# Kernel optimization log

Hardware: AMD Instinct MI355X
Metric: run time of the kernel (lower is better)

Reference implementation:

```python
import jax, jax.numpy as jnp
import numpy as np

N, C, H, W = 8, 64, 256, 256
HO, WO = 256, 256


def setup_inputs() -> dict:
    key = jax.random.key(0)
    kx, kg = jax.random.split(key)
    x = jax.random.normal(kx, (N, C, H, W), dtype=jnp.float32)
    # normalized sampling coords in [-1, 1], last dim = (x, y)
    grid = jax.random.uniform(kg, (N, HO, WO, 2), dtype=jnp.float32, minval=-1.0, maxval=1.0)
    return {"x": x, "grid": grid}


def reference(x, grid):
    # Bilinear grid sample, align_corners=True, border-clamped indices
    # x: [N, C, H, W]; grid: [N, Ho, Wo, 2] in [-1, 1]
    n, c, h, w = x.shape
    ix = (grid[..., 0] + 1.0) * 0.5 * (w - 1)  # [N, Ho, Wo] unnormalized x coord
    iy = (grid[..., 1] + 1.0) * 0.5 * (h - 1)

    x0f = jnp.floor(ix)
    y0f = jnp.floor(iy)
    wx1 = ix - x0f  # frac weights
    wy1 = iy - y0f
    wx0 = 1.0 - wx1
    wy0 = 1.0 - wy1

    x0 = jnp.clip(x0f, 0, w - 1).astype(jnp.int32)
    x1 = jnp.clip(x0f + 1.0, 0, w - 1).astype(jnp.int32)
    y0 = jnp.clip(y0f, 0, h - 1).astype(jnp.int32)
    y1 = jnp.clip(y0f + 1.0, 0, h - 1).astype(jnp.int32)

    xt = jnp.transpose(x, (0, 2, 3, 1))  # [N, H, W, C] for channels-last gather
    b = jnp.arange(n)[:, None, None]  # [N, 1, 1] batch index

    def gather(yi, xi):
        return xt[b, yi, xi]  # [N, Ho, Wo, C]

    out = (gather(y0, x0) * (wy0 * wx0)[..., None]
           + gather(y0, x1) * (wy0 * wx1)[..., None]
           + gather(y1, x0) * (wy1 * wx0)[..., None]
           + gather(y1, x1) * (wy1 * wx1)[..., None])
    return jnp.transpose(out, (0, 3, 1, 2))  # [N, C, Ho, Wo]
```

## Files before the change

kernel.cpp:

```cpp
#include <hip/hip_runtime.h>
#include <hip/hip_bf16.h>


constexpr int N = 8, C = 64, H = 256, W = 256, HO = 256, WO = 256;
constexpr int NPIX = N * HO * WO;
constexpr int PLANE = H * W;
constexpr size_t XT_BYTES = (size_t)N * C * PLANE * sizeof(float);

__global__ __launch_bounds__(256) void transpose_kernel(
    const float* __restrict__ x, float* __restrict__ xt) {
  __shared__ float tile[64][65];
  int tx = threadIdx.x;
  int ty = threadIdx.y;
  int tileIdx = blockIdx.x;
  int n = tileIdx >> 10;
  int pixb = (tileIdx & 1023) << 6;

  const float* xn = x + (size_t)n * C * PLANE;
#pragma unroll
  for (int k = 0; k < 16; ++k) {
    int c = (k << 2) + ty;
    tile[c][tx] = __builtin_nontemporal_load(&xn[(size_t)c * PLANE + pixb + tx]);
  }
  __syncthreads();
  float* xtn = xt + ((size_t)n * PLANE + pixb) * C;
#pragma unroll
  for (int k = 0; k < 16; ++k) {
    int p = (k << 2) + ty;
    xtn[(size_t)p * C + tx] = tile[tx][p];
  }
}

__global__ __launch_bounds__(256) void sample_kernel(
    const float* __restrict__ xt, const float* __restrict__ grid,
    float* __restrict__ out) {
  __shared__ float tile[4][64][33];
  __shared__ float4 wts[4][64];
  __shared__ int bs[4][64];

  int lane = threadIdx.x & 63;
  int wid = threadIdx.x >> 6;
  int gwave = blockIdx.x * 4 + wid;
  int pixb = gwave << 6;
  int p_idx = pixb + lane;
  int n = p_idx >> 16;

  float2 g = ((const float2*)grid)[p_idx];
  float ix = (g.x + 1.0f) * 0.5f * (float)(W - 1);
  float iy = (g.y + 1.0f) * 0.5f * (float)(H - 1);
  float x0f = floorf(ix), y0f = floorf(iy);
  float fx = ix - x0f, fy = iy - y0f;
  float cx0 = fminf(fmaxf(x0f,        0.f), (float)(W - 1));
  float cx1 = fminf(fmaxf(x0f + 1.f,  0.f), (float)(W - 1));
  float cy0 = fminf(fmaxf(y0f,        0.f), (float)(H - 1));
  float cy1 = fminf(fmaxf(y0f + 1.f,  0.f), (float)(H - 1));
  int x0 = (int)cx0, x1 = (int)cx1, y0 = (int)cy0, y1 = (int)cy1;
  int xl = min(x0, W - 2), yl = min(y0, H - 2);
  float wx0 = 1.f - fx, wx1 = fx, wy0 = 1.f - fy, wy1 = fy;
  float wxl = (x0 == xl ? wx0 : 0.f) + (x1 == xl ? wx1 : 0.f);
  float wxh = (x0 == xl + 1 ? wx0 : 0.f) + (x1 == xl + 1 ? wx1 : 0.f);
  float wyl = (y0 == yl ? wy0 : 0.f) + (y1 == yl ? wy1 : 0.f);
  float wyh = (y0 == yl + 1 ? wy0 : 0.f) + (y1 == yl + 1 ? wy1 : 0.f);
  wts[wid][lane] = make_float4(wyl * wxl, wyl * wxh, wyh * wxl, wyh * wxh);
  bs[wid][lane] = ((n << 16) | (yl << 8) | xl) << 6;
  __syncthreads();

  int prow = pixb & (PLANE - 1);
  float* outn = out + (size_t)n * C * PLANE + prow;

  for (int h = 0; h < 2; ++h) {
#pragma unroll 4
    for (int q = 0; q < 32; ++q) {
      int p = (h << 5) + q;
      float4 wv = wts[wid][p];
      const float* src = xt + bs[wid][p] + lane;
      float a = src[0];
      float b = src[C];
      float cv = src[C * W];
      float d = src[C * W + C];
      tile[wid][lane][q] = a * wv.x + b * wv.y + cv * wv.z + d * wv.w;
    }
    __syncthreads();
    int pq = lane & 31;
    int cbase = lane >> 5;
#pragma unroll 8
    for (int k = 0; k < 32; ++k) {
      int c = (k << 1) + cbase;
      __builtin_nontemporal_store(tile[wid][c][pq],
                                  &outn[(size_t)c * PLANE + (h << 5) + pq]);
    }
    __syncthreads();
  }
}

__global__ __launch_bounds__(256) void grid_sample_fallback(
    const float* __restrict__ x, const float* __restrict__ grid,
    float* __restrict__ out) {
  int idx = blockIdx.x * blockDim.x + threadIdx.x;
  if (idx >= NPIX) return;
  int wo = idx & (WO - 1);
  int ho = (idx >> 8) & (HO - 1);
  int n  = idx >> 16;
  float2 g = ((const float2*)grid)[idx];
  float ix = (g.x + 1.0f) * 0.5f * (float)(W - 1);
  float iy = (g.y + 1.0f) * 0.5f * (float)(H - 1);
  float x0f = floorf(ix), y0f = floorf(iy);
  float wx1 = ix - x0f, wy1 = iy - y0f;
  float wx0 = 1.0f - wx1, wy0 = 1.0f - wy1;
  int x0 = (int)fminf(fmaxf(x0f,        0.0f), (float)(W - 1));
  int x1 = (int)fminf(fmaxf(x0f + 1.0f, 0.0f), (float)(W - 1));
  int y0 = (int)fminf(fmaxf(y0f,        0.0f), (float)(H - 1));
  int y1 = (int)fminf(fmaxf(y0f + 1.0f, 0.0f), (float)(H - 1));
  float w00 = wy0 * wx0, w01 = wy0 * wx1, w10 = wy1 * wx0, w11 = wy1 * wx1;
  int o00 = y0 * W + x0, o01 = y0 * W + x1, o10 = y1 * W + x0, o11 = y1 * W + x1;
  const float* xn = x + (size_t)n * C * PLANE;
  float* on = out + (size_t)n * C * PLANE + (size_t)ho * WO + wo;
#pragma unroll 4
  for (int c = 0; c < C; ++c) {
    const float* xc = xn + c * PLANE;
    float v = xc[o00] * w00 + xc[o01] * w01 + xc[o10] * w10 + xc[o11] * w11;
    __builtin_nontemporal_store(v, on + (size_t)c * PLANE);
  }
}

extern "C" void kernel_launch(void* const* d_in, const int* in_sizes, int n_in,
                              void* d_out, int out_size, void* d_ws, size_t ws_size,
                              hipStream_t stream) {
  const float* x    = (const float*)d_in[0];
  const float* grid = (const float*)d_in[1];
  float* out        = (float*)d_out;

  if (ws_size >= XT_BYTES) {
    float* xt = (float*)d_ws;
    transpose_kernel<<<N * PLANE / 64, dim3(64, 4), 0, stream>>>(x, xt);
    sample_kernel<<<NPIX / 256, 256, 0, stream>>>(xt, grid, out);
  } else {
    grid_sample_fallback<<<NPIX / 256, 256, 0, stream>>>(x, grid, out);
  }
}
```

Before: 302.4 us.

## Store channels-last intermediate in bf16 and use single-wave sample blocks

The transpose kernel now writes the channels-last copy of x as packed bf16 pairs instead of fp32, halving intermediate write and gather read traffic. The sample kernel reads bf16 and widens to fp32 before the bilinear blend. It also switches to one 64-thread block per 64 pixels, dropping the 4-wave block, and unrolls the gather loop deeper. Rounding inputs to bf16 reduces accuracy, roughly 3 significant digits, which may breach tolerance.

```diff
diff --git a/kernel.cpp b/kernel.cpp
--- a/kernel.cpp
+++ b/kernel.cpp
@@ -5,13 +5,20 @@
 constexpr int N = 8, C = 64, H = 256, W = 256, HO = 256, WO = 256;
 constexpr int NPIX = N * HO * WO;
 constexpr int PLANE = H * W;
-constexpr size_t XT_BYTES = (size_t)N * C * PLANE * sizeof(float);
+constexpr size_t XT_BYTES = (size_t)N * PLANE * C * sizeof(unsigned short);
+
+__device__ __forceinline__ float bf16_to_f(unsigned short u) {
+  union { unsigned int i; float f; } v;
+  v.i = ((unsigned int)u) << 16;
+  return v.f;
+}
 
 __global__ __launch_bounds__(256) void transpose_kernel(
-    const float* __restrict__ x, float* __restrict__ xt) {
+    const float* __restrict__ x, unsigned int* __restrict__ xt) {
   __shared__ float tile[64][65];
   int tx = threadIdx.x;
   int ty = threadIdx.y;
+  int t = (ty << 6) + tx;
   int tileIdx = blockIdx.x;
   int n = tileIdx >> 10;
   int pixb = (tileIdx & 1023) << 6;
@@ -23,25 +30,30 @@
     tile[c][tx] = __builtin_nontemporal_load(&xn[(size_t)c * PLANE + pixb + tx]);
   }
   __syncthreads();
-  float* xtn = xt + ((size_t)n * PLANE + pixb) * C;
+
+  unsigned int* xtw = xt + ((size_t)(n * PLANE + pixb)) * 32;
+  int chp = t & 31;
 #pragma unroll
-  for (int k = 0; k < 16; ++k) {
-    int p = (k << 2) + ty;
-    xtn[(size_t)p * C + tx] = tile[tx][p];
+  for (int k = 0; k < 8; ++k) {
+    int p = (k << 3) + (t >> 5);
+    float f0 = tile[2 * chp][p];
+    float f1 = tile[2 * chp + 1][p];
+    __hip_bfloat162 h2 = __float22bfloat162_rn(make_float2(f0, f1));
+    unsigned int w;
+    __builtin_memcpy(&w, &h2, 4);
+    xtw[(size_t)p * 32 + chp] = w;
   }
 }
 
-__global__ __launch_bounds__(256) void sample_kernel(
-    const float* __restrict__ xt, const float* __restrict__ grid,
+__global__ __launch_bounds__(64) void sample_kernel(
+    const unsigned short* __restrict__ xt, const float* __restrict__ grid,
     float* __restrict__ out) {
-  __shared__ float tile[4][64][33];
-  __shared__ float4 wts[4][64];
-  __shared__ int bs[4][64];
+  __shared__ float tile[64][33];
+  __shared__ float4 wts[64];
+  __shared__ int bs[64];
 
-  int lane = threadIdx.x & 63;
-  int wid = threadIdx.x >> 6;
-  int gwave = blockIdx.x * 4 + wid;
-  int pixb = gwave << 6;
+  int lane = threadIdx.x;
+  int pixb = blockIdx.x << 6;
   int p_idx = pixb + lane;
   int n = p_idx >> 16;
 
@@ -61,32 +73,32 @@
   float wxh = (x0 == xl + 1 ? wx0 : 0.f) + (x1 == xl + 1 ? wx1 : 0.f);
   float wyl = (y0 == yl ? wy0 : 0.f) + (y1 == yl ? wy1 : 0.f);
   float wyh = (y0 == yl + 1 ? wy0 : 0.f) + (y1 == yl + 1 ? wy1 : 0.f);
-  wts[wid][lane] = make_float4(wyl * wxl, wyl * wxh, wyh * wxl, wyh * wxh);
-  bs[wid][lane] = ((n << 16) | (yl << 8) | xl) << 6;
+  wts[lane] = make_float4(wyl * wxl, wyl * wxh, wyh * wxl, wyh * wxh);
+  bs[lane] = ((n << 16) | (yl << 8) | xl) << 6;
   __syncthreads();
 
   int prow = pixb & (PLANE - 1);
   float* outn = out + (size_t)n * C * PLANE + prow;
 
   for (int h = 0; h < 2; ++h) {
-#pragma unroll 4
+#pragma unroll 8
     for (int q = 0; q < 32; ++q) {
       int p = (h << 5) + q;
-      float4 wv = wts[wid][p];
-      const float* src = xt + bs[wid][p] + lane;
-      float a = src[0];
-      float b = src[C];
-      float cv = src[C * W];
-      float d = src[C * W + C];
-      tile[wid][lane][q] = a * wv.x + b * wv.y + cv * wv.z + d * wv.w;
+      float4 wv = wts[p];
+      const unsigned short* src = xt + bs[p] + lane;
+      float a  = bf16_to_f(src[0]);
+      float b  = bf16_to_f(src[C]);
+      float cv = bf16_to_f(src[C * W]);
+      float d  = bf16_to_f(src[C * W + C]);
+      tile[lane][q] = a * wv.x + b * wv.y + cv * wv.z + d * wv.w;
     }
     __syncthreads();
     int pq = lane & 31;
-    int cbase = lane >> 5;
+    int cb = lane >> 5;
 #pragma unroll 8
     for (int k = 0; k < 32; ++k) {
-      int c = (k << 1) + cbase;
-      __builtin_nontemporal_store(tile[wid][c][pq],
+      int c = (k << 1) + cb;
+      __builtin_nontemporal_store(tile[c][pq],
                                   &outn[(size_t)c * PLANE + (h << 5) + pq]);
     }
     __syncthreads();
@@ -131,9 +143,10 @@
   float* out        = (float*)d_out;
 
   if (ws_size >= XT_BYTES) {
-    float* xt = (float*)d_ws;
-    transpose_kernel<<<N * PLANE / 64, dim3(64, 4), 0, stream>>>(x, xt);
-    sample_kernel<<<NPIX / 256, 256, 0, stream>>>(xt, grid, out);
+    transpose_kernel<<<N * PLANE / 64, dim3(64, 4), 0, stream>>>(
+        x, (unsigned int*)d_ws);
+    sample_kernel<<<NPIX / 64, 64, 0, stream>>>(
+        (const unsigned short*)d_ws, grid, out);
   } else {
     grid_sample_fallback<<<NPIX / 256, 256, 0, stream>>>(x, grid, out);
   }
```

Measured after the change: 276.5 us. 1.09x faster.
